# Optimization experiments

Measured on AMD Instinct MI355X. Metric: run time of the kernel, lower is better.

The kernel has to match this reference:

```python
import jax, jax.numpy as jnp
import numpy as np

NEG_FILL = -9e15  # matches torch masked_fill value

def setup_inputs() -> dict:
    key = jax.random.key(0)
    k1, k2, k3 = jax.random.split(key, 3)
    shape = (1, 16, 4096, 64)  # [batch, heads, seq, d_head]
    q = jax.random.normal(k1, shape, dtype=jnp.float32)
    k = jax.random.normal(k2, shape, dtype=jnp.float32)
    v = jax.random.normal(k3, shape, dtype=jnp.float32)
    return {"q": q, "k": k, "v": v}

def reference(q, k, v):
    d_k = q.shape[-1]
    S_q, S_k = q.shape[-2], k.shape[-2]
    # scores: [b, h, s_q, s_k]
    scores = jnp.einsum('bhqd,bhkd->bhqk', q, k) / jnp.sqrt(jnp.float32(d_k))
    # causal mask (lower triangular allowed)
    causal = jnp.tril(jnp.ones((S_q, S_k), dtype=bool))
    scores = jnp.where(causal, scores, jnp.float32(NEG_FILL))
    attn = jax.nn.softmax(scores, axis=-1)
    return jnp.einsum('bhqk,bhkd->bhqd', attn, v)
```

## Files before the change

kernel.cpp:

```cpp
#include <hip/hip_runtime.h>

#define SS 4096
#define DD 64
#define NH 16
#define QB 128
#define NQB (SS / QB)
#define KVT 64
#define NKV (SS / KVT)
#define TILE_BYTES 8192

#define CHUNKS_PER_H 144
#define ACCW_PER_H   112
#define LM_PLANE     (16 * CHUNKS_PER_H * 128)

typedef float  fx4    __attribute__((ext_vector_type(4)));
typedef __bf16 bf16x8 __attribute__((ext_vector_type(8)));
typedef short  sx4    __attribute__((ext_vector_type(4)));
typedef unsigned short usx4 __attribute__((ext_vector_type(4)));

typedef __attribute__((address_space(1))) const unsigned int GU32;
typedef __attribute__((address_space(3))) unsigned int       LU32;

__device__ __forceinline__ void gload16(const void* g, void* l) {
    __builtin_amdgcn_global_load_lds((GU32*)g, (LU32*)l, 16, 0, 0);
}

__device__ __forceinline__ float fast_exp2(float x) {
    return __builtin_amdgcn_exp2f(x);
}

__global__ __launch_bounds__(256)
void prep_kernel(const float* __restrict__ Kg, const float* __restrict__ Vg,
                 char* __restrict__ Kimg, char* __restrict__ Vimg)
{
    __shared__ __bf16 lv[64][72];
    const int tid = threadIdx.x;
    const int h = (int)blockIdx.x >> 6;
    const int t = (int)blockIdx.x & 63;
    const int r = tid >> 2;
    const size_t rowbase = ((size_t)h * SS + (size_t)t * KVT) * DD;

    {
        char* kdst = Kimg + (size_t)(h * NKV + t) * TILE_BYTES;
        const float* src = Kg + rowbase + (size_t)r * DD;
#pragma unroll
        for (int cc = 0; cc < 2; ++cc) {
            const int c = (tid & 3) * 2 + cc;
            fx4 f0 = *(const fx4*)(src + c * 8);
            fx4 f1 = *(const fx4*)(src + c * 8 + 4);
            bf16x8 b;
#pragma unroll
            for (int j = 0; j < 4; ++j) { b[j] = (__bf16)f0[j]; b[4 + j] = (__bf16)f1[j]; }
            *(bf16x8*)(kdst + r * 128 + ((c ^ (r & 7)) << 4)) = b;
        }
    }

    {
        const float* src = Vg + rowbase + (size_t)r * DD + (tid & 3) * 16;
#pragma unroll
        for (int qq = 0; qq < 4; ++qq) {
            fx4 f = *(const fx4*)(src + qq * 4);
#pragma unroll
            for (int j = 0; j < 4; ++j) lv[r][(tid & 3) * 16 + qq * 4 + j] = (__bf16)f[j];
        }
    }
    __syncthreads();
    {
        char* vdst = Vimg + (size_t)(h * NKV + t) * TILE_BYTES;
        const int d = r;
#pragma unroll
        for (int cc = 0; cc < 2; ++cc) {
            const int c = (tid & 3) * 2 + cc;
            bf16x8 b;
#pragma unroll
            for (int j = 0; j < 8; ++j) b[j] = lv[c * 8 + j][d];
            *(bf16x8*)(vdst + d * 128 + ((c ^ (d & 7)) << 4)) = b;
        }
    }
}

__global__ __launch_bounds__(256, 4)
void attn_fwd(const float* __restrict__ Qg, const char* __restrict__ Kimg,
              const char* __restrict__ Vimg, float* __restrict__ Og,
              unsigned short* __restrict__ accW, float* __restrict__ lmW)
{
    __shared__ __align__(16) char lK[2][TILE_BYTES];
    __shared__ __align__(16) char lV[2][TILE_BYTES];

    const int tid  = threadIdx.x;
    const int wid  = tid >> 6;
    const int lane = tid & 63;
    const int lr   = lane & 15;
    const int g    = lane >> 4;

    const int b = (int)blockIdx.x;
    const int h = b / CHUNKS_PER_H;
    int r_ = (CHUNKS_PER_H - 1) - (b - h * CHUNKS_PER_H);
    const int cid = r_;
    int m = 0;
#pragma unroll
    for (int i = 0; i < 7; ++i) {
        if (r_ >= 4 * (i + 1)) { r_ -= 4 * (i + 1); m = i + 1; }
    }
    int p4 = 0;
#pragma unroll
    for (int i = 0; i < 3; ++i) {
        if (r_ >= m + 1) { r_ -= (m + 1); ++p4; }
    }
    const int p  = 4 * m + p4;
    const int ci = r_;
    const int n  = m + 1;
    const int W  = 2 * p + 2;
    const int t0 = (ci * W) / n;
    const int t1 = ((ci + 1) * W) / n;

    const int q0 = p * QB + wid * 32;

    const float* Qh = Qg + (size_t)h * SS * DD;
    float*       Oh = Og + (size_t)h * SS * DD;
    const char*  Kh = Kimg + (size_t)(h * NKV) * TILE_BYTES;
    const char*  Vh = Vimg + (size_t)(h * NKV) * TILE_BYTES;

    const float QSCALE = 0.125f * 1.44269504088896f;

    bf16x8 qa[2][2];
#pragma unroll
    for (int u = 0; u < 2; ++u) {
        const int qrow = q0 + 16 * u + lr;
#pragma unroll
        for (int h2 = 0; h2 < 2; ++h2) {
            const float* src = Qh + (size_t)qrow * DD + h2 * 32 + g * 8;
            fx4 f0 = *(const fx4*)(src);
            fx4 f1 = *(const fx4*)(src + 4);
            bf16x8 tq;
#pragma unroll
            for (int jj = 0; jj < 4; ++jj) {
                tq[jj]     = (__bf16)(f0[jj] * QSCALE);
                tq[jj + 4] = (__bf16)(f1[jj] * QSCALE);
            }
            qa[u][h2] = tq;
        }
    }

    fx4 acc[2][4];
#pragma unroll
    for (int u = 0; u < 2; ++u)
#pragma unroll
        for (int d0 = 0; d0 < 4; ++d0) acc[u][d0] = (fx4){0.f, 0.f, 0.f, 0.f};
    float m_run = -1e30f;
    float l_run[2] = {0.f, 0.f};

#define STAGE(buf, tt)                                                          \
    do {                                                                        \
        const char* img_ = (wid < 2) ? Kh : Vh;                                 \
        char* dst_ = ((wid < 2) ? &lK[buf][0] : &lV[buf][0]) + (wid & 1) * 4096;\
        const char* src_ = img_ + (size_t)(tt) * TILE_BYTES + (wid & 1) * 4096  \
                           + lane * 16;                                         \
        gload16(src_,        dst_);                                             \
        gload16(src_ + 1024, dst_ + 1024);                                      \
        gload16(src_ + 2048, dst_ + 2048);                                      \
        gload16(src_ + 3072, dst_ + 3072);                                      \
    } while (0)

    STAGE(0, t0);
    __syncthreads();

    int cur = 0;
    for (int t = t0; t < t1; ++t) {
        if (t + 1 < t1) STAGE(cur ^ 1, t + 1);

        float s[2][4][4];
        __builtin_amdgcn_s_setprio(1);
#pragma unroll
        for (int ks = 0; ks < 4; ++ks) {
            const int row = ks * 16 + lr;
            const char* base = &lK[cur][row * 128];
            const bf16x8 ka0 = *(const bf16x8*)(base + (((g    ) ^ (row & 7)) << 4));
            const bf16x8 ka1 = *(const bf16x8*)(base + (((g ^ 4) ^ (row & 7)) << 4));
#pragma unroll
            for (int u = 0; u < 2; ++u) {
                fx4 st = (fx4){0.f, 0.f, 0.f, 0.f};
                st = __builtin_amdgcn_mfma_f32_16x16x32_bf16(ka0, qa[u][0], st, 0, 0, 0);
                st = __builtin_amdgcn_mfma_f32_16x16x32_bf16(ka1, qa[u][1], st, 0, 0, 0);
#pragma unroll
                for (int r = 0; r < 4; ++r) s[u][ks][r] = st[r];
            }
        }
        __builtin_amdgcn_s_setprio(0);

        if (t >= 2 * p) {
            const int kv0 = t * KVT;
#pragma unroll
            for (int u = 0; u < 2; ++u) {
                const int qrow = q0 + 16 * u + lr;
#pragma unroll
                for (int ks = 0; ks < 4; ++ks)
#pragma unroll
                    for (int r = 0; r < 4; ++r) {
                        const int kvi = kv0 + ks * 16 + 4 * g + r;
                        if (kvi > qrow) s[u][ks][r] = -1e30f;
                    }
            }
        }

        float m4[2][4];
#pragma unroll
        for (int u = 0; u < 2; ++u)
#pragma unroll
            for (int ks = 0; ks < 4; ++ks)
                m4[u][ks] = fmaxf(fmaxf(s[u][ks][0], s[u][ks][1]),
                                  fmaxf(s[u][ks][2], s[u][ks][3]));
        const float tm = fmaxf(
            fmaxf(fmaxf(m4[0][0], m4[0][1]), fmaxf(m4[0][2], m4[0][3])),
            fmaxf(fmaxf(m4[1][0], m4[1][1]), fmaxf(m4[1][2], m4[1][3])));

        if (__any(tm > m_run + 8.0f)) {
            float wm = tm;
            wm = fmaxf(wm, __shfl_xor(wm, 1));
            wm = fmaxf(wm, __shfl_xor(wm, 2));
            wm = fmaxf(wm, __shfl_xor(wm, 4));
            wm = fmaxf(wm, __shfl_xor(wm, 8));
            wm = fmaxf(wm, __shfl_xor(wm, 16));
            wm = fmaxf(wm, __shfl_xor(wm, 32));
            const float alpha = fast_exp2(m_run - wm);
            m_run = wm;
            l_run[0] *= alpha; l_run[1] *= alpha;
#pragma unroll
            for (int u = 0; u < 2; ++u)
#pragma unroll
                for (int d0 = 0; d0 < 4; ++d0) {
                    fx4 a = acc[u][d0];
                    a[0] *= alpha; a[1] *= alpha; a[2] *= alpha; a[3] *= alpha;
                    acc[u][d0] = a;
                }
        }

        sx4 pa[2][4];
#pragma unroll
        for (int u = 0; u < 2; ++u) {
            float e[4][4];
#pragma unroll
            for (int ks = 0; ks < 4; ++ks)
#pragma unroll
                for (int r = 0; r < 4; ++r)
                    e[ks][r] = fast_exp2(s[u][ks][r] - m_run);
            const float u0 = (e[0][0] + e[0][1]) + (e[0][2] + e[0][3]);
            const float u1 = (e[1][0] + e[1][1]) + (e[1][2] + e[1][3]);
            const float u2 = (e[2][0] + e[2][1]) + (e[2][2] + e[2][3]);
            const float u3 = (e[3][0] + e[3][1]) + (e[3][2] + e[3][3]);
            l_run[u] += (u0 + u1) + (u2 + u3);
#pragma unroll
            for (int ks = 0; ks < 4; ++ks) {
                sx4 t4;
#pragma unroll
                for (int jj = 0; jj < 4; ++jj) {
                    const __bf16 pb = (__bf16)e[ks][jj];
                    t4[jj] = __builtin_bit_cast(short, pb);
                }
                pa[u][ks] = t4;
            }
        }

        __builtin_amdgcn_s_setprio(1);
#pragma unroll
        for (int ks = 0; ks < 4; ++ks) {
            const int s0 = ks * 2 + (g >> 1);
#pragma unroll
            for (int d0 = 0; d0 < 4; ++d0) {
                const int row = d0 * 16 + lr;
                const sx4 vb = *(const sx4*)(&lV[cur][row * 128 +
                                ((s0 ^ (row & 7)) << 4) + (g & 1) * 8]);
                acc[0][d0] = __builtin_amdgcn_mfma_f32_16x16x16bf16_1k(pa[0][ks], vb, acc[0][d0], 0, 0, 0);
                acc[1][d0] = __builtin_amdgcn_mfma_f32_16x16x16bf16_1k(pa[1][ks], vb, acc[1][d0], 0, 0, 0);
            }
        }
        __builtin_amdgcn_s_setprio(0);

        if (t + 1 < t1) __syncthreads();
        cur ^= 1;
    }

    float ls0 = l_run[0];
    ls0 += __shfl_xor(ls0, 16);
    ls0 += __shfl_xor(ls0, 32);
    float ls1 = l_run[1];
    ls1 += __shfl_xor(ls1, 16);
    ls1 += __shfl_xor(ls1, 32);

    const int rowb = (h * CHUNKS_PER_H + cid) * 128 + wid * 32 + lr;
    if (lane < 16) {
        lmW[rowb]                = m_run;
        lmW[rowb + 16]           = m_run;
        lmW[LM_PLANE + rowb]       = ls0;
        lmW[LM_PLANE + rowb + 16]  = ls1;
    }

    if (ci == 0) {
#pragma unroll
        for (int u = 0; u < 2; ++u)
#pragma unroll
            for (int d0 = 0; d0 < 4; ++d0)
#pragma unroll
                for (int r = 0; r < 4; ++r)
                    Oh[(size_t)(q0 + 16 * u + 4 * g + r) * DD + d0 * 16 + lr] = acc[u][d0][r];
    } else {
        const size_t ab = ((size_t)(h * ACCW_PER_H) + (cid - p - 1)) * 8192
                        + (size_t)(wid * 32) * 64;
#pragma unroll
        for (int u = 0; u < 2; ++u)
#pragma unroll
            for (int d0 = 0; d0 < 4; ++d0)
#pragma unroll
                for (int r = 0; r < 4; ++r) {
                    const __bf16 pb = (__bf16)acc[u][d0][r];
                    accW[ab + (size_t)(16 * u + 4 * g + r) * 64 + d0 * 16 + lr] =
                        __builtin_bit_cast(unsigned short, pb);
                }
    }
#undef STAGE
}

__global__ __launch_bounds__(256)
void combine_kernel(float* __restrict__ Og, const unsigned short* __restrict__ accW,
                    const float* __restrict__ lmW)
{
    const int blk = (int)blockIdx.x;
    const int rg = blk & 7;
    const int p  = (blk >> 3) & 31;
    const int h  = blk >> 8;

    const int m = p >> 2, n = m + 1;
    const int cid0 = 2 * m * (m + 1) + (p & 3) * n;
    const int lmB  = (h * CHUNKS_PER_H + cid0) * 128;
    const size_t obase = ((size_t)h * SS + (size_t)p * QB) * DD;
    const size_t ab0   = ((size_t)(h * ACCW_PER_H) + (cid0 - p)) * 8192;

    const int row = rg * 16 + ((int)threadIdx.x >> 4);
    const int c4  = ((int)threadIdx.x & 15) * 4;

    float mi[8], li[8];
#pragma unroll
    for (int i = 0; i < 8; ++i) {
        const int ic = (i < n) ? i : 0;
        mi[i] = lmW[lmB + ic * 128 + row];
        li[i] = lmW[LM_PLANE + lmB + ic * 128 + row];
    }
#pragma unroll
    for (int i = 0; i < 8; ++i) {
        if (i >= n) { mi[i] = -3.0e38f; li[i] = 0.f; }
    }
    const float mm = fmaxf(fmaxf(fmaxf(mi[0], mi[1]), fmaxf(mi[2], mi[3])),
                           fmaxf(fmaxf(mi[4], mi[5]), fmaxf(mi[6], mi[7])));
    float w[8];
    float den = 0.f;
#pragma unroll
    for (int i = 0; i < 8; ++i) {
        w[i] = fast_exp2(mi[i] - mm);
        den += w[i] * li[i];
    }

    const size_t oi = obase + (size_t)row * DD + c4;
    fx4 val = *(const fx4*)(&Og[oi]);
    val[0] *= w[0]; val[1] *= w[0]; val[2] *= w[0]; val[3] *= w[0];

#pragma unroll
    for (int i = 1; i < 8; ++i) {
        const int ai = (i < n) ? (i - 1) : 0;
        const usx4 ub = *(const usx4*)(&accW[ab0 + (size_t)ai * 8192 + row * 64 + c4]);
#pragma unroll
        for (int j = 0; j < 4; ++j) {
            const unsigned int bits = ((unsigned int)ub[j]) << 16;
            val[j] += w[i] * __builtin_bit_cast(float, bits);
        }
    }

    const float rinv = 1.f / den;
    val[0] *= rinv; val[1] *= rinv; val[2] *= rinv; val[3] *= rinv;
    *(fx4*)(&Og[oi]) = val;
}

extern "C" void kernel_launch(void* const* d_in, const int* in_sizes, int n_in,
                              void* d_out, int out_size, void* d_ws, size_t ws_size,
                              hipStream_t stream)
{
    (void)in_sizes; (void)n_in; (void)out_size; (void)ws_size;
    const float* q = (const float*)d_in[0];
    const float* k = (const float*)d_in[1];
    const float* v = (const float*)d_in[2];
    float*       o = (float*)d_out;

    char* ws = (char*)d_ws;
    char*           Kimg = ws;
    char*           Vimg = ws + ((size_t)1 << 23);
    unsigned short* accW = (unsigned short*)(ws + ((size_t)2 << 23));
    float*          lmW  = (float*)(ws + ((size_t)2 << 23) + 29360128);

    hipLaunchKernelGGL(prep_kernel,    dim3(NH * NKV),          dim3(256), 0, stream, k, v, Kimg, Vimg);
    hipLaunchKernelGGL(attn_fwd,       dim3(NH * CHUNKS_PER_H), dim3(256), 0, stream, q, Kimg, Vimg, o, accW, lmW);
    hipLaunchKernelGGL(combine_kernel, dim3(4096),              dim3(256), 0, stream, o, accW, lmW);
}
```

Baseline: 86.92 us.

## Load V tiles directly from global into registers, staging only K in LDS

Stops staging the V image through shared memory. Each wave now reads its V operand fragments straight from global (L2) into registers after the QK^T MFMAs, and the V image is written unswizzled to suit this. This halves LDS use and the async copy work per tile, which may allow more resident blocks. The cost is global-load latency on the critical path before the PV MFMAs, with nothing prefetching it. Smaller tweaks precompute the swizzled K LDS offsets, reuse the score registers for the exponentials, and reshape the max-reduction tree.

```diff
diff --git a/kernel.cpp b/kernel.cpp
--- a/kernel.cpp
+++ b/kernel.cpp
@@ -74,7 +74,7 @@
             bf16x8 b;
 #pragma unroll
             for (int j = 0; j < 8; ++j) b[j] = lv[c * 8 + j][d];
-            *(bf16x8*)(vdst + d * 128 + ((c ^ (d & 7)) << 4)) = b;
+            *(bf16x8*)(vdst + d * 128 + (c << 4)) = b;
         }
     }
 }
@@ -85,7 +85,6 @@
               unsigned short* __restrict__ accW, float* __restrict__ lmW)
 {
     __shared__ __align__(16) char lK[2][TILE_BYTES];
-    __shared__ __align__(16) char lV[2][TILE_BYTES];
 
     const int tid  = threadIdx.x;
     const int wid  = tid >> 6;
@@ -123,6 +122,15 @@
 
     const float QSCALE = 0.125f * 1.44269504088896f;
 
+    int koff[4][2];
+#pragma unroll
+    for (int ks = 0; ks < 4; ++ks) {
+        const int row = ks * 16 + lr;
+        koff[ks][0] = row * 128 + (((g    ) ^ (lr & 7)) << 4);
+        koff[ks][1] = row * 128 + (((g ^ 4) ^ (lr & 7)) << 4);
+    }
+    const int vbase = lr * 128 + g * 8;
+
     bf16x8 qa[2][2];
 #pragma unroll
     for (int u = 0; u < 2; ++u) {
@@ -152,14 +160,11 @@
 
 #define STAGE(buf, tt)                                                          \
     do {                                                                        \
-        const char* img_ = (wid < 2) ? Kh : Vh;                                 \
-        char* dst_ = ((wid < 2) ? &lK[buf][0] : &lV[buf][0]) + (wid & 1) * 4096;\
-        const char* src_ = img_ + (size_t)(tt) * TILE_BYTES + (wid & 1) * 4096  \
+        const char* src_ = Kh + (size_t)(tt) * TILE_BYTES + wid * 2048          \
                            + lane * 16;                                         \
+        char* dst_ = &lK[buf][wid * 2048];                                      \
         gload16(src_,        dst_);                                             \
         gload16(src_ + 1024, dst_ + 1024);                                      \
-        gload16(src_ + 2048, dst_ + 2048);                                      \
-        gload16(src_ + 3072, dst_ + 3072);                                      \
     } while (0)
 
     STAGE(0, t0);
@@ -170,13 +175,12 @@
         if (t + 1 < t1) STAGE(cur ^ 1, t + 1);
 
         float s[2][4][4];
+        const char* kb = &lK[cur][0];
         __builtin_amdgcn_s_setprio(1);
 #pragma unroll
         for (int ks = 0; ks < 4; ++ks) {
-            const int row = ks * 16 + lr;
-            const char* base = &lK[cur][row * 128];
-            const bf16x8 ka0 = *(const bf16x8*)(base + (((g    ) ^ (row & 7)) << 4));
-            const bf16x8 ka1 = *(const bf16x8*)(base + (((g ^ 4) ^ (row & 7)) << 4));
+            const bf16x8 ka0 = *(const bf16x8*)(kb + koff[ks][0]);
+            const bf16x8 ka1 = *(const bf16x8*)(kb + koff[ks][1]);
 #pragma unroll
             for (int u = 0; u < 2; ++u) {
                 fx4 st = (fx4){0.f, 0.f, 0.f, 0.f};
@@ -187,6 +191,16 @@
             }
         }
         __builtin_amdgcn_s_setprio(0);
+
+        sx4 vbr[4][4];
+        {
+            const char* vt = Vh + (size_t)t * TILE_BYTES + vbase;
+#pragma unroll
+            for (int ks = 0; ks < 4; ++ks)
+#pragma unroll
+                for (int d0 = 0; d0 < 4; ++d0)
+                    vbr[ks][d0] = *(const sx4*)(vt + d0 * 2048 + ks * 32);
+        }
 
         if (t >= 2 * p) {
             const int kv0 = t * KVT;
@@ -210,9 +224,10 @@
             for (int ks = 0; ks < 4; ++ks)
                 m4[u][ks] = fmaxf(fmaxf(s[u][ks][0], s[u][ks][1]),
                                   fmaxf(s[u][ks][2], s[u][ks][3]));
-        const float tm = fmaxf(
-            fmaxf(fmaxf(m4[0][0], m4[0][1]), fmaxf(m4[0][2], m4[0][3])),
-            fmaxf(fmaxf(m4[1][0], m4[1][1]), fmaxf(m4[1][2], m4[1][3])));
+        const float ta = fmaxf(fmaxf(m4[0][0], m4[0][1]), m4[0][2]);
+        const float tb = fmaxf(fmaxf(m4[0][3], m4[1][0]), m4[1][1]);
+        const float tc = fmaxf(fmaxf(m4[1][2], m4[1][3]), ta);
+        const float tm = fmaxf(tb, tc);
 
         if (__any(tm > m_run + 8.0f)) {
             float wm = tm;
@@ -238,23 +253,22 @@
         sx4 pa[2][4];
 #pragma unroll
         for (int u = 0; u < 2; ++u) {
-            float e[4][4];
 #pragma unroll
             for (int ks = 0; ks < 4; ++ks)
 #pragma unroll
                 for (int r = 0; r < 4; ++r)
-                    e[ks][r] = fast_exp2(s[u][ks][r] - m_run);
-            const float u0 = (e[0][0] + e[0][1]) + (e[0][2] + e[0][3]);
-            const float u1 = (e[1][0] + e[1][1]) + (e[1][2] + e[1][3]);
-            const float u2 = (e[2][0] + e[2][1]) + (e[2][2] + e[2][3]);
-            const float u3 = (e[3][0] + e[3][1]) + (e[3][2] + e[3][3]);
+                    s[u][ks][r] = fast_exp2(s[u][ks][r] - m_run);
+            const float u0 = (s[u][0][0] + s[u][0][1]) + (s[u][0][2] + s[u][0][3]);
+            const float u1 = (s[u][1][0] + s[u][1][1]) + (s[u][1][2] + s[u][1][3]);
+            const float u2 = (s[u][2][0] + s[u][2][1]) + (s[u][2][2] + s[u][2][3]);
+            const float u3 = (s[u][3][0] + s[u][3][1]) + (s[u][3][2] + s[u][3][3]);
             l_run[u] += (u0 + u1) + (u2 + u3);
 #pragma unroll
             for (int ks = 0; ks < 4; ++ks) {
                 sx4 t4;
 #pragma unroll
                 for (int jj = 0; jj < 4; ++jj) {
-                    const __bf16 pb = (__bf16)e[ks][jj];
+                    const __bf16 pb = (__bf16)s[u][ks][jj];
                     t4[jj] = __builtin_bit_cast(short, pb);
                 }
                 pa[u][ks] = t4;
@@ -264,14 +278,10 @@
         __builtin_amdgcn_s_setprio(1);
 #pragma unroll
         for (int ks = 0; ks < 4; ++ks) {
-            const int s0 = ks * 2 + (g >> 1);
 #pragma unroll
             for (int d0 = 0; d0 < 4; ++d0) {
-                const int row = d0 * 16 + lr;
-                const sx4 vb = *(const sx4*)(&lV[cur][row * 128 +
-                                ((s0 ^ (row & 7)) << 4) + (g & 1) * 8]);
-                acc[0][d0] = __builtin_amdgcn_mfma_f32_16x16x16bf16_1k(pa[0][ks], vb, acc[0][d0], 0, 0, 0);
-                acc[1][d0] = __builtin_amdgcn_mfma_f32_16x16x16bf16_1k(pa[1][ks], vb, acc[1][d0], 0, 0, 0);
+                acc[0][d0] = __builtin_amdgcn_mfma_f32_16x16x16bf16_1k(pa[0][ks], vbr[ks][d0], acc[0][d0], 0, 0, 0);
+                acc[1][d0] = __builtin_amdgcn_mfma_f32_16x16x16bf16_1k(pa[1][ks], vbr[ks][d0], acc[1][d0], 0, 0, 0);
             }
         }
         __builtin_amdgcn_s_setprio(0);
@@ -289,8 +299,8 @@
 
     const int rowb = (h * CHUNKS_PER_H + cid) * 128 + wid * 32 + lr;
     if (lane < 16) {
-        lmW[rowb]                = m_run;
-        lmW[rowb + 16]           = m_run;
+        lmW[rowb]                  = m_run;
+        lmW[rowb + 16]             = m_run;
         lmW[LM_PLANE + rowb]       = ls0;
         lmW[LM_PLANE + rowb + 16]  = ls1;
     }
```

Result: slower. 241.7 us (+178.0%).

## Split attention block into 8 waves of 16 query rows each

Applied to the files above, without the earlier changes.

The attention block now has 8 waves of 512 threads. Each wave owns 16 query rows instead of 32, so per-thread Q fragments, accumulators and score registers are halved. K/V tile staging is spread over all 8 waves with two loads each. The intent is more resident waves per CU to hide latency, at the cost of each K/V fragment read from LDS feeding half as many MFMAs, which lowers reuse and adds block-wide sync cost.

```diff
diff --git a/kernel.cpp b/kernel.cpp
--- a/kernel.cpp
+++ b/kernel.cpp
@@ -79,7 +79,7 @@
     }
 }
 
-__global__ __launch_bounds__(256, 4)
+__global__ __launch_bounds__(512, 8)
 void attn_fwd(const float* __restrict__ Qg, const char* __restrict__ Kimg,
               const char* __restrict__ Vimg, float* __restrict__ Og,
               unsigned short* __restrict__ accW, float* __restrict__ lmW)
@@ -114,7 +114,7 @@
     const int t0 = (ci * W) / n;
     const int t1 = ((ci + 1) * W) / n;
 
-    const int q0 = p * QB + wid * 32;
+    const int q0 = p * QB + wid * 16;
 
     const float* Qh = Qg + (size_t)h * SS * DD;
     float*       Oh = Og + (size_t)h * SS * DD;
@@ -123,10 +123,9 @@
 
     const float QSCALE = 0.125f * 1.44269504088896f;
 
-    bf16x8 qa[2][2];
-#pragma unroll
-    for (int u = 0; u < 2; ++u) {
-        const int qrow = q0 + 16 * u + lr;
+    bf16x8 qa[2];
+    {
+        const int qrow = q0 + lr;
 #pragma unroll
         for (int h2 = 0; h2 < 2; ++h2) {
             const float* src = Qh + (size_t)qrow * DD + h2 * 32 + g * 8;
@@ -138,28 +137,24 @@
                 tq[jj]     = (__bf16)(f0[jj] * QSCALE);
                 tq[jj + 4] = (__bf16)(f1[jj] * QSCALE);
             }
-            qa[u][h2] = tq;
-        }
-    }
-
-    fx4 acc[2][4];
-#pragma unroll
-    for (int u = 0; u < 2; ++u)
-#pragma unroll
-        for (int d0 = 0; d0 < 4; ++d0) acc[u][d0] = (fx4){0.f, 0.f, 0.f, 0.f};
+            qa[h2] = tq;
+        }
+    }
+
+    fx4 acc[4];
+#pragma unroll
+    for (int d0 = 0; d0 < 4; ++d0) acc[d0] = (fx4){0.f, 0.f, 0.f, 0.f};
     float m_run = -1e30f;
-    float l_run[2] = {0.f, 0.f};
+    float l_run = 0.f;
 
 #define STAGE(buf, tt)                                                          \
     do {                                                                        \
-        const char* img_ = (wid < 2) ? Kh : Vh;                                 \
-        char* dst_ = ((wid < 2) ? &lK[buf][0] : &lV[buf][0]) + (wid & 1) * 4096;\
-        const char* src_ = img_ + (size_t)(tt) * TILE_BYTES + (wid & 1) * 4096  \
-                           + lane * 16;                                         \
+        const int sw_ = wid & 3;                                                \
+        const char* src_ = ((wid < 4) ? Kh : Vh) + (size_t)(tt) * TILE_BYTES    \
+                           + sw_ * 2048 + lane * 16;                            \
+        char* dst_ = ((wid < 4) ? &lK[buf][0] : &lV[buf][0]) + sw_ * 2048;      \
         gload16(src_,        dst_);                                             \
         gload16(src_ + 1024, dst_ + 1024);                                      \
-        gload16(src_ + 2048, dst_ + 2048);                                      \
-        gload16(src_ + 3072, dst_ + 3072);                                      \
     } while (0)
 
     STAGE(0, t0);
@@ -169,7 +164,7 @@
     for (int t = t0; t < t1; ++t) {
         if (t + 1 < t1) STAGE(cur ^ 1, t + 1);
 
-        float s[2][4][4];
+        float s[4][4];
         __builtin_amdgcn_s_setprio(1);
 #pragma unroll
         for (int ks = 0; ks < 4; ++ks) {
@@ -177,42 +172,31 @@
             const char* base = &lK[cur][row * 128];
             const bf16x8 ka0 = *(const bf16x8*)(base + (((g    ) ^ (row & 7)) << 4));
             const bf16x8 ka1 = *(const bf16x8*)(base + (((g ^ 4) ^ (row & 7)) << 4));
-#pragma unroll
-            for (int u = 0; u < 2; ++u) {
-                fx4 st = (fx4){0.f, 0.f, 0.f, 0.f};
-                st = __builtin_amdgcn_mfma_f32_16x16x32_bf16(ka0, qa[u][0], st, 0, 0, 0);
-                st = __builtin_amdgcn_mfma_f32_16x16x32_bf16(ka1, qa[u][1], st, 0, 0, 0);
-#pragma unroll
-                for (int r = 0; r < 4; ++r) s[u][ks][r] = st[r];
-            }
+            fx4 st = (fx4){0.f, 0.f, 0.f, 0.f};
+            st = __builtin_amdgcn_mfma_f32_16x16x32_bf16(ka0, qa[0], st, 0, 0, 0);
+            st = __builtin_amdgcn_mfma_f32_16x16x32_bf16(ka1, qa[1], st, 0, 0, 0);
+#pragma unroll
+            for (int r = 0; r < 4; ++r) s[ks][r] = st[r];
         }
         __builtin_amdgcn_s_setprio(0);
 
         if (t >= 2 * p) {
             const int kv0 = t * KVT;
-#pragma unroll
-            for (int u = 0; u < 2; ++u) {
-                const int qrow = q0 + 16 * u + lr;
-#pragma unroll
-                for (int ks = 0; ks < 4; ++ks)
-#pragma unroll
-                    for (int r = 0; r < 4; ++r) {
-                        const int kvi = kv0 + ks * 16 + 4 * g + r;
-                        if (kvi > qrow) s[u][ks][r] = -1e30f;
-                    }
-            }
-        }
-
-        float m4[2][4];
-#pragma unroll
-        for (int u = 0; u < 2; ++u)
+            const int qrow = q0 + lr;
 #pragma unroll
             for (int ks = 0; ks < 4; ++ks)
-                m4[u][ks] = fmaxf(fmaxf(s[u][ks][0], s[u][ks][1]),
-                                  fmaxf(s[u][ks][2], s[u][ks][3]));
+#pragma unroll
+                for (int r = 0; r < 4; ++r) {
+                    const int kvi = kv0 + ks * 16 + 4 * g + r;
+                    if (kvi > qrow) s[ks][r] = -1e30f;
+                }
+        }
+
         const float tm = fmaxf(
-            fmaxf(fmaxf(m4[0][0], m4[0][1]), fmaxf(m4[0][2], m4[0][3])),
-            fmaxf(fmaxf(m4[1][0], m4[1][1]), fmaxf(m4[1][2], m4[1][3])));
+            fmaxf(fmaxf(fmaxf(s[0][0], s[0][1]), fmaxf(s[0][2], s[0][3])),
+                  fmaxf(fmaxf(s[1][0], s[1][1]), fmaxf(s[1][2], s[1][3]))),
+            fmaxf(fmaxf(fmaxf(s[2][0], s[2][1]), fmaxf(s[2][2], s[2][3])),
+                  fmaxf(fmaxf(s[3][0], s[3][1]), fmaxf(s[3][2], s[3][3]))));
 
         if (__any(tm > m_run + 8.0f)) {
             float wm = tm;
@@ -224,40 +208,36 @@
             wm = fmaxf(wm, __shfl_xor(wm, 32));
             const float alpha = fast_exp2(m_run - wm);
             m_run = wm;
-            l_run[0] *= alpha; l_run[1] *= alpha;
-#pragma unroll
-            for (int u = 0; u < 2; ++u)
-#pragma unroll
-                for (int d0 = 0; d0 < 4; ++d0) {
-                    fx4 a = acc[u][d0];
-                    a[0] *= alpha; a[1] *= alpha; a[2] *= alpha; a[3] *= alpha;
-                    acc[u][d0] = a;
-                }
-        }
-
-        sx4 pa[2][4];
-#pragma unroll
-        for (int u = 0; u < 2; ++u) {
-            float e[4][4];
+            l_run *= alpha;
+#pragma unroll
+            for (int d0 = 0; d0 < 4; ++d0) {
+                fx4 a = acc[d0];
+                a[0] *= alpha; a[1] *= alpha; a[2] *= alpha; a[3] *= alpha;
+                acc[d0] = a;
+            }
+        }
+
+        sx4 pa[4];
+        {
 #pragma unroll
             for (int ks = 0; ks < 4; ++ks)
 #pragma unroll
                 for (int r = 0; r < 4; ++r)
-                    e[ks][r] = fast_exp2(s[u][ks][r] - m_run);
-            const float u0 = (e[0][0] + e[0][1]) + (e[0][2] + e[0][3]);
-            const float u1 = (e[1][0] + e[1][1]) + (e[1][2] + e[1][3]);
-            const float u2 = (e[2][0] + e[2][1]) + (e[2][2] + e[2][3]);
-            const float u3 = (e[3][0] + e[3][1]) + (e[3][2] + e[3][3]);
-            l_run[u] += (u0 + u1) + (u2 + u3);
+                    s[ks][r] = fast_exp2(s[ks][r] - m_run);
+            const float u0 = (s[0][0] + s[0][1]) + (s[0][2] + s[0][3]);
+            const float u1 = (s[1][0] + s[1][1]) + (s[1][2] + s[1][3]);
+            const float u2 = (s[2][0] + s[2][1]) + (s[2][2] + s[2][3]);
+            const float u3 = (s[3][0] + s[3][1]) + (s[3][2] + s[3][3]);
+            l_run += (u0 + u1) + (u2 + u3);
 #pragma unroll
             for (int ks = 0; ks < 4; ++ks) {
                 sx4 t4;
 #pragma unroll
                 for (int jj = 0; jj < 4; ++jj) {
-                    const __bf16 pb = (__bf16)e[ks][jj];
+                    const __bf16 pb = (__bf16)s[ks][jj];
                     t4[jj] = __builtin_bit_cast(short, pb);
                 }
-                pa[u][ks] = t4;
+                pa[ks] = t4;
             }
         }
 
@@ -270,8 +250,7 @@
                 const int row = d0 * 16 + lr;
                 const sx4 vb = *(const sx4*)(&lV[cur][row * 128 +
                                 ((s0 ^ (row & 7)) << 4) + (g & 1) * 8]);
-                acc[0][d0] = __builtin_amdgcn_mfma_f32_16x16x16bf16_1k(pa[0][ks], vb, acc[0][d0], 0, 0, 0);
-                acc[1][d0] = __builtin_amdgcn_mfma_f32_16x16x16bf16_1k(pa[1][ks], vb, acc[1][d0], 0, 0, 0);
+                acc[d0] = __builtin_amdgcn_mfma_f32_16x16x16bf16_1k(pa[ks], vb, acc[d0], 0, 0, 0);
             }
         }
         __builtin_amdgcn_s_setprio(0);
@@ -280,42 +259,33 @@
         cur ^= 1;
     }
 
-    float ls0 = l_run[0];
-    ls0 += __shfl_xor(ls0, 16);
-    ls0 += __shfl_xor(ls0, 32);
-    float ls1 = l_run[1];
-    ls1 += __shfl_xor(ls1, 16);
-    ls1 += __shfl_xor(ls1, 32);
-
-    const int rowb = (h * CHUNKS_PER_H + cid) * 128 + wid * 32 + lr;
+    float ls = l_run;
+    ls += __shfl_xor(ls, 16);
+    ls += __shfl_xor(ls, 32);
+
+    const int rowb = (h * CHUNKS_PER_H + cid) * 128 + wid * 16 + lr;
     if (lane < 16) {
-        lmW[rowb]                = m_run;
-        lmW[rowb + 16]           = m_run;
-        lmW[LM_PLANE + rowb]       = ls0;
-        lmW[LM_PLANE + rowb + 16]  = ls1;
+        lmW[rowb]            = m_run;
+        lmW[LM_PLANE + rowb] = ls;
     }
 
     if (ci == 0) {
 #pragma unroll
-        for (int u = 0; u < 2; ++u)
-#pragma unroll
-            for (int d0 = 0; d0 < 4; ++d0)
-#pragma unroll
-                for (int r = 0; r < 4; ++r)
-                    Oh[(size_t)(q0 + 16 * u + 4 * g + r) * DD + d0 * 16 + lr] = acc[u][d0][r];
+        for (int d0 = 0; d0 < 4; ++d0)
+#pragma unroll
+            for (int r = 0; r < 4; ++r)
+                Oh[(size_t)(q0 + 4 * g + r) * DD + d0 * 16 + lr] = acc[d0][r];
     } else {
         const size_t ab = ((size_t)(h * ACCW_PER_H) + (cid - p - 1)) * 8192
-                        + (size_t)(wid * 32) * 64;
-#pragma unroll
-        for (int u = 0; u < 2; ++u)
-#pragma unroll
-            for (int d0 = 0; d0 < 4; ++d0)
-#pragma unroll
-                for (int r = 0; r < 4; ++r) {
-                    const __bf16 pb = (__bf16)acc[u][d0][r];
-                    accW[ab + (size_t)(16 * u + 4 * g + r) * 64 + d0 * 16 + lr] =
-                        __builtin_bit_cast(unsigned short, pb);
-                }
+                        + (size_t)(wid * 16) * 64;
+#pragma unroll
+        for (int d0 = 0; d0 < 4; ++d0)
+#pragma unroll
+            for (int r = 0; r < 4; ++r) {
+                const __bf16 pb = (__bf16)acc[d0][r];
+                accW[ab + (size_t)(4 * g + r) * 64 + d0 * 16 + lr] =
+                    __builtin_bit_cast(unsigned short, pb);
+            }
     }
 #undef STAGE
 }
@@ -396,6 +366,6 @@
     float*          lmW  = (float*)(ws + ((size_t)2 << 23) + 29360128);
 
     hipLaunchKernelGGL(prep_kernel,    dim3(NH * NKV),          dim3(256), 0, stream, k, v, Kimg, Vimg);
-    hipLaunchKernelGGL(attn_fwd,       dim3(NH * CHUNKS_PER_H), dim3(256), 0, stream, q, Kimg, Vimg, o, accW, lmW);
+    hipLaunchKernelGGL(attn_fwd,       dim3(NH * CHUNKS_PER_H), dim3(512), 0, stream, q, Kimg, Vimg, o, accW, lmW);
     hipLaunchKernelGGL(combine_kernel, dim3(4096),              dim3(256), 0, stream, o, accW, lmW);
 }
```

Result: slower. 115.9 us (+33.3%).

## Triple-buffer K/V tiles with prefetch distance two and explicit vmcnt barriers

Applied to the files above, without the earlier changes.

Grows the K/V shared-memory ring from two to three buffers and issues global-to-LDS loads two tiles ahead. The full __syncthreads is replaced by s_waitcnt vmcnt(4) plus s_barrier, so only the older tile has to arrive and one tile's loads stay in flight across the barrier. The intent is to hide more global memory latency behind MFMA work. The cost is more LDS per block and lowering launch bounds from 4 to 3 blocks per CU, which reduces occupancy. The exp values are also written back into the score array to save registers.

```diff
diff --git a/kernel.cpp b/kernel.cpp
--- a/kernel.cpp
+++ b/kernel.cpp
@@ -79,13 +79,13 @@
     }
 }
 
-__global__ __launch_bounds__(256, 4)
+__global__ __launch_bounds__(256, 3)
 void attn_fwd(const float* __restrict__ Qg, const char* __restrict__ Kimg,
               const char* __restrict__ Vimg, float* __restrict__ Og,
               unsigned short* __restrict__ accW, float* __restrict__ lmW)
 {
-    __shared__ __align__(16) char lK[2][TILE_BYTES];
-    __shared__ __align__(16) char lV[2][TILE_BYTES];
+    __shared__ __align__(16) char lK[3][TILE_BYTES];
+    __shared__ __align__(16) char lV[3][TILE_BYTES];
 
     const int tid  = threadIdx.x;
     const int wid  = tid >> 6;
@@ -163,11 +163,18 @@
     } while (0)
 
     STAGE(0, t0);
-    __syncthreads();
+    if (t0 + 1 < t1) {
+        STAGE(1, t0 + 1);
+        asm volatile("s_waitcnt vmcnt(4)\n\ts_barrier" ::: "memory");
+    } else {
+        asm volatile("s_waitcnt vmcnt(0)\n\ts_barrier" ::: "memory");
+    }
+    __builtin_amdgcn_sched_barrier(0);
 
     int cur = 0;
     for (int t = t0; t < t1; ++t) {
-        if (t + 1 < t1) STAGE(cur ^ 1, t + 1);
+        const int nx2 = (cur >= 1) ? cur - 1 : cur + 2;
+        if (t + 2 < t1) STAGE(nx2, t + 2);
 
         float s[2][4][4];
         __builtin_amdgcn_s_setprio(1);
@@ -238,23 +245,22 @@
         sx4 pa[2][4];
 #pragma unroll
         for (int u = 0; u < 2; ++u) {
-            float e[4][4];
 #pragma unroll
             for (int ks = 0; ks < 4; ++ks)
 #pragma unroll
                 for (int r = 0; r < 4; ++r)
-                    e[ks][r] = fast_exp2(s[u][ks][r] - m_run);
-            const float u0 = (e[0][0] + e[0][1]) + (e[0][2] + e[0][3]);
-            const float u1 = (e[1][0] + e[1][1]) + (e[1][2] + e[1][3]);
-            const float u2 = (e[2][0] + e[2][1]) + (e[2][2] + e[2][3]);
-            const float u3 = (e[3][0] + e[3][1]) + (e[3][2] + e[3][3]);
+                    s[u][ks][r] = fast_exp2(s[u][ks][r] - m_run);
+            const float u0 = (s[u][0][0] + s[u][0][1]) + (s[u][0][2] + s[u][0][3]);
+            const float u1 = (s[u][1][0] + s[u][1][1]) + (s[u][1][2] + s[u][1][3]);
+            const float u2 = (s[u][2][0] + s[u][2][1]) + (s[u][2][2] + s[u][2][3]);
+            const float u3 = (s[u][3][0] + s[u][3][1]) + (s[u][3][2] + s[u][3][3]);
             l_run[u] += (u0 + u1) + (u2 + u3);
 #pragma unroll
             for (int ks = 0; ks < 4; ++ks) {
                 sx4 t4;
 #pragma unroll
                 for (int jj = 0; jj < 4; ++jj) {
-                    const __bf16 pb = (__bf16)e[ks][jj];
+                    const __bf16 pb = (__bf16)s[u][ks][jj];
                     t4[jj] = __builtin_bit_cast(short, pb);
                 }
                 pa[u][ks] = t4;
@@ -276,8 +282,15 @@
         }
         __builtin_amdgcn_s_setprio(0);
 
-        if (t + 1 < t1) __syncthreads();
-        cur ^= 1;
+        if (t + 1 < t1) {
+            __builtin_amdgcn_sched_barrier(0);
+            if (t + 2 < t1)
+                asm volatile("s_waitcnt vmcnt(4)\n\ts_barrier" ::: "memory");
+            else
+                asm volatile("s_waitcnt vmcnt(0)\n\ts_barrier" ::: "memory");
+            __builtin_amdgcn_sched_barrier(0);
+        }
+        cur = (cur == 2) ? 0 : cur + 1;
     }
 
     float ls0 = l_run[0];
@@ -289,8 +302,8 @@
 
     const int rowb = (h * CHUNKS_PER_H + cid) * 128 + wid * 32 + lr;
     if (lane < 16) {
-        lmW[rowb]                = m_run;
-        lmW[rowb + 16]           = m_run;
+        lmW[rowb]                  = m_run;
+        lmW[rowb + 16]             = m_run;
         lmW[LM_PLANE + rowb]       = ls0;
         lmW[LM_PLANE + rowb + 16]  = ls1;
     }
```

New measurement: 88.89 us. 1.02x slower.
